# Kernel tuning notes

Hardware: AMD Instinct MI355X
Metric: run time of the kernel (lower is better)

The kernel has to match this reference:

```python
import jax, jax.numpy as jnp
import numpy as np

N_NODES = 50000
N_EDGES = 600000
N_GRAPHS = 512
D_IN = 128
D_H = 128
D_OUT = 10
N_LAYERS = 3
BN_EPS = 1e-5


def setup_inputs() -> dict:
    key = jax.random.key(0)
    ks = jax.random.split(key, 16)
    x = jax.random.normal(ks[0], (N_NODES, D_IN), dtype=jnp.float32)
    edge_index = jax.random.randint(ks[1], (2, N_EDGES), 0, N_NODES)
    # deterministic sorted batch assignment -> every graph non-empty
    batch = (jnp.arange(N_NODES) * N_GRAPHS) // N_NODES
    s = 1.0 / np.sqrt(D_H)
    w_in = jax.random.normal(ks[2], (D_IN, D_H), dtype=jnp.float32) * s
    b_in = jnp.zeros((D_H,), jnp.float32)
    conv_w = jax.random.normal(ks[3], (N_LAYERS, D_H, D_H), dtype=jnp.float32) * s
    conv_b = jnp.zeros((N_LAYERS, D_H), jnp.float32)
    bn_g = jnp.ones((N_LAYERS, D_H), jnp.float32)
    bn_b = jnp.zeros((N_LAYERS, D_H), jnp.float32)
    fc1_w = jax.random.normal(ks[4], (2 * D_H, D_H), dtype=jnp.float32) * (1.0 / np.sqrt(2 * D_H))
    fc1_b = jnp.zeros((D_H,), jnp.float32)
    fc2_w = jax.random.normal(ks[5], (D_H, D_OUT), dtype=jnp.float32) * s
    fc2_b = jnp.zeros((D_OUT,), jnp.float32)
    return {"x": x, "edge_index": edge_index, "batch": batch, "n_graphs": N_GRAPHS,
            "w_in": w_in, "b_in": b_in, "conv_w": conv_w, "conv_b": conv_b,
            "bn_g": bn_g, "bn_b": bn_b, "fc1_w": fc1_w, "fc1_b": fc1_b,
            "fc2_w": fc2_w, "fc2_b": fc2_b}


def reference(x, edge_index, batch, n_graphs, w_in, b_in, conv_w, conv_b,
              bn_g, bn_b, fc1_w, fc1_b, fc2_w, fc2_b):
    n = x.shape[0]
    loop = jnp.arange(n)
    src = jnp.concatenate([edge_index[0], loop])  # self-loops as in PyG GCNConv
    dst = jnp.concatenate([edge_index[1], loop])
    deg = jax.ops.segment_sum(jnp.ones_like(dst, x.dtype), dst, num_segments=n)
    dinv = jax.lax.rsqrt(deg)  # deg >= 1 due to self-loops
    enorm = dinv[src] * dinv[dst]  # (E+N,)

    h = jax.nn.relu(x @ w_in + b_in)
    for i in range(N_LAYERS):
        res = h
        m = h @ conv_w[i]
        # gather -> scale -> scatter-add (symmetric-normalized GCN propagation)
        m = jax.ops.segment_sum(m[src] * enorm[:, None], dst, num_segments=n) + conv_b[i]
        # batchnorm (training-mode batch statistics)
        mu = jnp.mean(m, axis=0)
        var = jnp.mean(jnp.square(m - mu), axis=0)
        m = (m - mu) * jax.lax.rsqrt(var + BN_EPS) * bn_g[i] + bn_b[i]
        m = jax.nn.relu(m)  # dropout is identity in eval
        h = m + res if i > 0 else m

    cnt = jax.ops.segment_sum(jnp.ones((n,), h.dtype), batch, num_segments=n_graphs)
    g_mean = jax.ops.segment_sum(h, batch, num_segments=n_graphs) / cnt[:, None]
    g_max = jax.ops.segment_max(h, batch, num_segments=n_graphs)
    g = jnp.concatenate([g_mean, g_max], axis=1)  # (G, 2*D_H)
    g = jax.nn.relu(g @ fc1_w + fc1_b)
    return g @ fc2_w + fc2_b
```

## Files before the change

### kernel.cpp

```cpp
#include <hip/hip_runtime.h>
#include <hip/hip_bf16.h>
#include <hip/hip_fp16.h>

#define N_NODES 50000
#define N_EDGES 600000
#define N_GRAPHS 512
#define DH 128
#define SLOTS 64
#define NCOPY 8

typedef __attribute__((ext_vector_type(8))) short bf16x8;
typedef __attribute__((ext_vector_type(4))) float fx4;
typedef __attribute__((ext_vector_type(8))) _Float16 hx8;

__device__ __forceinline__ short f2b(float f) {
    union { __hip_bfloat16 b; short s; } u;
    u.b = __float2bfloat16(f);
    return u.s;
}

__global__ void k_fill(const int* __restrict__ src, const int* __restrict__ dst,
                       int* __restrict__ fill, int* __restrict__ csr) {
    int e = blockIdx.x * 256 + threadIdx.x;
    if (e < N_EDGES) {
        int v = dst[e];
        int pos = atomicAdd(&fill[v], 1);
        if (pos < SLOTS) csr[v * SLOTS + pos] = src[e];
    }
}

__global__ void k_dinv(const int* __restrict__ fill, float* __restrict__ dinv) {
    int v = blockIdx.x * 256 + threadIdx.x;
    if (v < N_NODES) dinv[v] = rsqrtf((float)(fill[v] + 1));
}

__global__ void k_wcvt(const float* __restrict__ w_in, const float* __restrict__ conv_w,
                       __hip_bfloat16* __restrict__ Wp) {
    int id = blockIdx.x * 256 + threadIdx.x;
    if (id >= 4 * DH * DH) return;
    int mat = id >> 14, rem = id & 16383;
    int n = rem >> 7, k = rem & 127;
    const float* s = (mat == 0) ? w_in : (conv_w + (mat - 1) * DH * DH);
    Wp[id] = __float2bfloat16(s[k * DH + n]);
}

template <int MODE>
__global__ __launch_bounds__(256) void k_gemm(const float* __restrict__ A,
                                              const __hip_bfloat16* __restrict__ Wp,
                                              const float* __restrict__ bias,
                                              const float* __restrict__ coef,
                                              float* __restrict__ Hout,
                                              void* __restrict__ Cv) {
    int wave = blockIdx.x * 4 + (threadIdx.x >> 6);
    if (wave >= N_NODES / 16) return;
    int lane = threadIdx.x & 63;
    int r = lane & 15, gq = lane >> 4;
    const int row0 = wave * 16;

    const short* wp = (const short*)Wp;
    bf16x8 Bf[8][4];
#pragma unroll
    for (int t = 0; t < 8; ++t)
#pragma unroll
        for (int q = 0; q < 4; ++q)
            Bf[t][q] = *(const bf16x8*)(wp + (t * 16 + r) * DH + q * 32 + gq * 8);

    fx4 acc[8];
#pragma unroll
    for (int t = 0; t < 8; ++t) acc[t] = (fx4){0.f, 0.f, 0.f, 0.f};

    const float* arow = A + (size_t)(row0 + r) * DH;
#pragma unroll
    for (int q = 0; q < 4; ++q) {
        const int cb = q * 32 + gq * 8;
        fx4 a0 = *(const fx4*)(arow + cb);
        fx4 a1 = *(const fx4*)(arow + cb + 4);
        if (MODE >= 2) {
            fx4 sA0 = *(const fx4*)(coef + cb);
            fx4 sA1 = *(const fx4*)(coef + cb + 4);
            fx4 sB0 = *(const fx4*)(coef + DH + cb);
            fx4 sB1 = *(const fx4*)(coef + DH + cb + 4);
#pragma unroll
            for (int j = 0; j < 4; ++j) {
                a0[j] = fmaxf(a0[j] * sA0[j] + sB0[j], 0.f);
                a1[j] = fmaxf(a1[j] * sA1[j] + sB1[j], 0.f);
            }
            if (MODE == 3) {
                float* hrow = Hout + (size_t)(row0 + r) * DH + cb;
                a0 += *(const fx4*)(hrow);
                a1 += *(const fx4*)(hrow + 4);
            }
            float* hrow = Hout + (size_t)(row0 + r) * DH + cb;
            *(fx4*)(hrow) = a0;
            *(fx4*)(hrow + 4) = a1;
        }
        bf16x8 af;
        af[0] = f2b(a0[0]); af[1] = f2b(a0[1]); af[2] = f2b(a0[2]); af[3] = f2b(a0[3]);
        af[4] = f2b(a1[0]); af[5] = f2b(a1[1]); af[6] = f2b(a1[2]); af[7] = f2b(a1[3]);
#pragma unroll
        for (int t = 0; t < 8; ++t)
            acc[t] = __builtin_amdgcn_mfma_f32_16x16x32_bf16(af, Bf[t][q], acc[t], 0, 0, 0);
    }
#pragma unroll
    for (int t = 0; t < 8; ++t) {
#pragma unroll
        for (int rr = 0; rr < 4; ++rr) {
            int orow = row0 + 4 * gq + rr;
            int ocol = t * 16 + r;
            float v = acc[t][rr];
            if (MODE == 0) {
                v += bias[ocol];
                ((float*)Cv)[(size_t)orow * DH + ocol] = fmaxf(v, 0.f);
            } else {
                ((_Float16*)Cv)[(size_t)orow * DH + ocol] = (_Float16)v;
            }
        }
    }
}

__global__ __launch_bounds__(256) void k_prop(const _Float16* __restrict__ m,
                                              const int* __restrict__ csr,
                                              const int* __restrict__ deg,
                                              const float* __restrict__ dinv,
                                              float* __restrict__ agg,
                                              float* __restrict__ sums) {
    int g = threadIdx.x >> 4;
    int lane = threadIdx.x & 15;
    int v = blockIdx.x * 16 + g;
    float dv = dinv[v];
    hx8 self = ((const hx8*)(m + (size_t)v * DH))[lane];
    float acc[8];
#pragma unroll
    for (int j = 0; j < 8; ++j) acc[j] = dv * (float)self[j];
    int d = deg[v]; if (d > SLOTS) d = SLOTS;
    const int* nb = csr + (size_t)v * SLOTS;
    int i = 0;
    for (; i + 1 < d; i += 2) {
        int u0 = nb[i], u1 = nb[i + 1];
        float d0 = dinv[u0], d1 = dinv[u1];
        hx8 r0 = ((const hx8*)(m + (size_t)u0 * DH))[lane];
        hx8 r1 = ((const hx8*)(m + (size_t)u1 * DH))[lane];
#pragma unroll
        for (int j = 0; j < 8; ++j) acc[j] += d0 * (float)r0[j] + d1 * (float)r1[j];
    }
    if (i < d) {
        int u = nb[i];
        float du = dinv[u];
        hx8 ru = ((const hx8*)(m + (size_t)u * DH))[lane];
#pragma unroll
        for (int j = 0; j < 8; ++j) acc[j] += du * (float)ru[j];
    }
    float s[8], q2[8];
#pragma unroll
    for (int j = 0; j < 8; ++j) {
        float o = dv * acc[j];
        acc[j] = o;
        s[j] = o;
        q2[j] = o * o;
    }
    fx4 o0, o1;
#pragma unroll
    for (int j = 0; j < 4; ++j) { o0[j] = acc[j]; o1[j] = acc[4 + j]; }
    fx4* orow = (fx4*)(agg + (size_t)v * DH);
    orow[lane * 2] = o0;
    orow[lane * 2 + 1] = o1;

#pragma unroll
    for (int j = 0; j < 8; ++j) {
        s[j] += __shfl_xor(s[j], 16);
        s[j] += __shfl_xor(s[j], 32);
        q2[j] += __shfl_xor(q2[j], 16);
        q2[j] += __shfl_xor(q2[j], 32);
    }
    __shared__ float lsum[4][DH], lsq[4][DH];
    int wv = threadIdx.x >> 6, wl = threadIdx.x & 63;
    if (wl < 16) {
#pragma unroll
        for (int j = 0; j < 8; ++j) {
            lsum[wv][wl * 8 + j] = s[j];
            lsq[wv][wl * 8 + j] = q2[j];
        }
    }
    __syncthreads();
    if (threadIdx.x < DH) {
        int c = threadIdx.x;
        float ts = lsum[0][c] + lsum[1][c] + lsum[2][c] + lsum[3][c];
        float tq = lsq[0][c] + lsq[1][c] + lsq[2][c] + lsq[3][c];
        float* dstp = sums + (blockIdx.x & (NCOPY - 1)) * 256;
        atomicAdd(&dstp[c], ts);
        atomicAdd(&dstp[DH + c], tq);
    }
}

__global__ void k_bnfin(const float* __restrict__ sums, const float* __restrict__ gamma,
                        const float* __restrict__ beta, float* __restrict__ coef) {
    int c = threadIdx.x;
    if (c >= DH) return;
    float s = 0.f, q = 0.f;
    for (int k = 0; k < NCOPY; ++k) { s += sums[k * 256 + c]; q += sums[k * 256 + DH + c]; }
    const float invn = 1.f / (float)N_NODES;
    float mean = s * invn;
    float var = q * invn - mean * mean;
    float sA = gamma[c] * rsqrtf(var + 1e-5f);
    coef[c] = sA;
    coef[DH + c] = beta[c] - mean * sA;
}

__global__ __launch_bounds__(256) void k_pool(const float* __restrict__ agg,
                                              const float* __restrict__ coef,
                                              const float* __restrict__ hres,
                                              float* __restrict__ g) {
    int gr = blockIdx.x;
    int start = (gr * N_NODES + N_GRAPHS - 1) / N_GRAPHS;
    int end = ((gr + 1) * N_NODES + N_GRAPHS - 1) / N_GRAPHS;
    int grp = threadIdx.x >> 5, c4 = threadIdx.x & 31;
    fx4 sA = ((const fx4*)coef)[c4];
    fx4 sB = ((const fx4*)(coef + DH))[c4];
    fx4 sm = (fx4){0.f, 0.f, 0.f, 0.f};
    fx4 mx = (fx4){-3.4e38f, -3.4e38f, -3.4e38f, -3.4e38f};
    for (int v = start + grp; v < end; v += 8) {
        fx4 a = ((const fx4*)(agg + (size_t)v * DH))[c4];
        fx4 r = ((const fx4*)(hres + (size_t)v * DH))[c4];
        fx4 hv;
#pragma unroll
        for (int j = 0; j < 4; ++j) hv[j] = fmaxf(a[j] * sA[j] + sB[j], 0.f) + r[j];
        sm += hv;
#pragma unroll
        for (int j = 0; j < 4; ++j) mx[j] = fmaxf(mx[j], hv[j]);
    }
    __shared__ fx4 lsm[8][32], lmx[8][32];
    lsm[grp][c4] = sm;
    lmx[grp][c4] = mx;
    __syncthreads();
    if (threadIdx.x < 32) {
        int c = threadIdx.x;
        fx4 tsm = lsm[0][c], tmx = lmx[0][c];
#pragma unroll
        for (int k = 1; k < 8; ++k) {
            tsm += lsm[k][c];
#pragma unroll
            for (int j = 0; j < 4; ++j) tmx[j] = fmaxf(tmx[j], lmx[k][c][j]);
        }
        float inv = 1.f / (float)(end - start);
        tsm *= inv;
        *(fx4*)(g + gr * 256 + c * 4) = tsm;
        *(fx4*)(g + gr * 256 + DH + c * 4) = tmx;
    }
}

__global__ void k_head(const float* __restrict__ g, const float* __restrict__ fc1w,
                       const float* __restrict__ fc1b, const float* __restrict__ fc2w,
                       const float* __restrict__ fc2b, float* __restrict__ out) {
    __shared__ float tt[DH];
    int gr = blockIdx.x, j = threadIdx.x;
    const float* grow = g + gr * 256;
    float acc = fc1b[j];
    for (int k = 0; k < 256; ++k) acc += grow[k] * fc1w[k * DH + j];
    tt[j] = fmaxf(acc, 0.f);
    __syncthreads();
    if (j < 10) {
        float o = fc2b[j];
        for (int k = 0; k < DH; ++k) o += tt[k] * fc2w[k * 10 + j];
        out[gr * 10 + j] = o;
    }
}

extern "C" void kernel_launch(void* const* d_in, const int* in_sizes, int n_in,
                              void* d_out, int out_size, void* d_ws, size_t ws_size,
                              hipStream_t stream) {
    const float* x      = (const float*)d_in[0];
    const int*   ei     = (const int*)d_in[1];
    const float* w_in   = (const float*)d_in[4];
    const float* b_in   = (const float*)d_in[5];
    const float* conv_w = (const float*)d_in[6];
    const float* bn_g   = (const float*)d_in[8];
    const float* bn_b   = (const float*)d_in[9];
    const float* fc1w   = (const float*)d_in[10];
    const float* fc1b   = (const float*)d_in[11];
    const float* fc2w   = (const float*)d_in[12];
    const float* fc2b   = (const float*)d_in[13];
    float* out = (float*)d_out;

    const int* e_src = ei;
    const int* e_dst = ei + N_EDGES;

    char* ws = (char*)d_ws;
    size_t o = 0;
    auto alloc = [&](size_t bytes) { size_t r = o; o += (bytes + 255) & ~(size_t)255; return r; };
    size_t o_fill   = alloc(N_NODES * 4);
    size_t o_bnsum  = alloc(3 * NCOPY * 256 * 4);
    size_t zero_end = o;
    size_t o_dinv   = alloc(N_NODES * 4);
    size_t o_csr    = alloc((size_t)N_NODES * SLOTS * 4);
    size_t o_coef   = alloc(3 * 256 * 4);
    size_t o_wp     = alloc(4 * DH * DH * 2);
    size_t o_g      = alloc(N_GRAPHS * 256 * 4);
    size_t o_h      = alloc((size_t)N_NODES * DH * 4);
    size_t o_m      = alloc((size_t)N_NODES * DH * 2);
    size_t o_agg    = alloc((size_t)N_NODES * DH * 4);
    (void)ws_size;

    int*   fill   = (int*)(ws + o_fill);
    float* bnsum  = (float*)(ws + o_bnsum);
    float* dinv   = (float*)(ws + o_dinv);
    int*   csr    = (int*)(ws + o_csr);
    float* coef   = (float*)(ws + o_coef);
    __hip_bfloat16* wp = (__hip_bfloat16*)(ws + o_wp);
    float* gbuf   = (float*)(ws + o_g);
    float* h      = (float*)(ws + o_h);
    _Float16* m   = (_Float16*)(ws + o_m);
    float* agg    = (float*)(ws + o_agg);

    hipMemsetAsync(ws, 0, zero_end, stream);

    k_fill<<<(N_EDGES + 255) / 256, 256, 0, stream>>>(e_src, e_dst, fill, csr);
    k_dinv<<<(N_NODES + 255) / 256, 256, 0, stream>>>(fill, dinv);
    k_wcvt<<<(4 * DH * DH + 255) / 256, 256, 0, stream>>>(w_in, conv_w, wp);

    const int gemm_blocks = (N_NODES / 16 + 3) / 4;

    k_gemm<0><<<gemm_blocks, 256, 0, stream>>>(x, wp, b_in, nullptr, nullptr, h);

    k_gemm<1><<<gemm_blocks, 256, 0, stream>>>(h, wp + 1 * DH * DH, nullptr, nullptr, nullptr, m);
    k_prop<<<N_NODES / 16, 256, 0, stream>>>(m, csr, fill, dinv, agg, bnsum);
    k_bnfin<<<1, DH, 0, stream>>>(bnsum, bn_g, bn_b, coef);

    k_gemm<2><<<gemm_blocks, 256, 0, stream>>>(agg, wp + 2 * DH * DH, nullptr, coef, h, m);
    k_prop<<<N_NODES / 16, 256, 0, stream>>>(m, csr, fill, dinv, agg, bnsum + NCOPY * 256);
    k_bnfin<<<1, DH, 0, stream>>>(bnsum + NCOPY * 256, bn_g + DH, bn_b + DH, coef + 256);

    k_gemm<3><<<gemm_blocks, 256, 0, stream>>>(agg, wp + 3 * DH * DH, nullptr, coef + 256, h, m);
    k_prop<<<N_NODES / 16, 256, 0, stream>>>(m, csr, fill, dinv, agg, bnsum + 2 * NCOPY * 256);
    k_bnfin<<<1, DH, 0, stream>>>(bnsum + 2 * NCOPY * 256, bn_g + 2 * DH, bn_b + 2 * DH, coef + 512);

    k_pool<<<N_GRAPHS, 256, 0, stream>>>(agg, coef + 512, h, gbuf);
    k_head<<<N_GRAPHS, DH, 0, stream>>>(gbuf, fc1w, fc1b, fc2w, fc2b, out);
}
```

Before: 351.2 us.

## Store h and agg in fp16, fold bnfin into prop, merge setup kernels

The intermediate node feature buffers h and agg switch from fp32 to fp16, which halves the memory traffic in the gemm, prop and pool kernels. The BN finalize step moves into the last block of each prop launch through an atomic ticket. The fill and weight-convert kernels merge into one launch, and dinv is now recomputed inline from the degrees. The prop gather is unrolled by 4 with int4 neighbour loads. The main costs are lower precision in the residual stream and extra rsqrt work per neighbour.

Result: slower. 1.215 ms (+245.8%).

```diff
diff --git a/kernel.cpp b/kernel.cpp
--- a/kernel.cpp
+++ b/kernel.cpp
@@ -8,6 +8,9 @@
 #define DH 128
 #define SLOTS 64
 #define NCOPY 8
+#define FILL_BLOCKS ((N_EDGES + 255) / 256)
+#define WCVT_BLOCKS ((4 * DH * DH) / 256)
+#define PROP_BLOCKS (N_NODES / 16)
 
 typedef __attribute__((ext_vector_type(8))) short bf16x8;
 typedef __attribute__((ext_vector_type(4))) float fx4;
@@ -19,38 +22,34 @@
     return u.s;
 }
 
-__global__ void k_fill(const int* __restrict__ src, const int* __restrict__ dst,
-                       int* __restrict__ fill, int* __restrict__ csr) {
-    int e = blockIdx.x * 256 + threadIdx.x;
-    if (e < N_EDGES) {
-        int v = dst[e];
-        int pos = atomicAdd(&fill[v], 1);
-        if (pos < SLOTS) csr[v * SLOTS + pos] = src[e];
-    }
-}
-
-__global__ void k_dinv(const int* __restrict__ fill, float* __restrict__ dinv) {
-    int v = blockIdx.x * 256 + threadIdx.x;
-    if (v < N_NODES) dinv[v] = rsqrtf((float)(fill[v] + 1));
-}
-
-__global__ void k_wcvt(const float* __restrict__ w_in, const float* __restrict__ conv_w,
-                       __hip_bfloat16* __restrict__ Wp) {
-    int id = blockIdx.x * 256 + threadIdx.x;
-    if (id >= 4 * DH * DH) return;
-    int mat = id >> 14, rem = id & 16383;
-    int n = rem >> 7, k = rem & 127;
-    const float* s = (mat == 0) ? w_in : (conv_w + (mat - 1) * DH * DH);
-    Wp[id] = __float2bfloat16(s[k * DH + n]);
+__global__ void k_build(const int* __restrict__ src, const int* __restrict__ dst,
+                        int* __restrict__ fill, int* __restrict__ csr,
+                        const float* __restrict__ w_in, const float* __restrict__ conv_w,
+                        __hip_bfloat16* __restrict__ Wp) {
+    int b = blockIdx.x;
+    if (b < FILL_BLOCKS) {
+        int e = b * 256 + threadIdx.x;
+        if (e < N_EDGES) {
+            int v = dst[e];
+            int pos = atomicAdd(&fill[v], 1);
+            if (pos < SLOTS) csr[v * SLOTS + pos] = src[e];
+        }
+    } else {
+        int id = (b - FILL_BLOCKS) * 256 + threadIdx.x;
+        int mat = id >> 14, rem = id & 16383;
+        int n = rem >> 7, k = rem & 127;
+        const float* s = (mat == 0) ? w_in : (conv_w + (mat - 1) * DH * DH);
+        Wp[id] = __float2bfloat16(s[k * DH + n]);
+    }
 }
 
 template <int MODE>
-__global__ __launch_bounds__(256) void k_gemm(const float* __restrict__ A,
+__global__ __launch_bounds__(256) void k_gemm(const void* __restrict__ Av,
                                               const __hip_bfloat16* __restrict__ Wp,
                                               const float* __restrict__ bias,
                                               const float* __restrict__ coef,
-                                              float* __restrict__ Hout,
-                                              void* __restrict__ Cv) {
+                                              _Float16* __restrict__ Hout,
+                                              _Float16* __restrict__ Cm) {
     int wave = blockIdx.x * 4 + (threadIdx.x >> 6);
     if (wave >= N_NODES / 16) return;
     int lane = threadIdx.x & 63;
@@ -69,12 +68,22 @@
 #pragma unroll
     for (int t = 0; t < 8; ++t) acc[t] = (fx4){0.f, 0.f, 0.f, 0.f};
 
-    const float* arow = A + (size_t)(row0 + r) * DH;
 #pragma unroll
     for (int q = 0; q < 4; ++q) {
         const int cb = q * 32 + gq * 8;
-        fx4 a0 = *(const fx4*)(arow + cb);
-        fx4 a1 = *(const fx4*)(arow + cb + 4);
+        float a[8];
+        if (MODE == 0) {
+            const float* arow = (const float*)Av + (size_t)(row0 + r) * DH + cb;
+            fx4 a0 = *(const fx4*)(arow);
+            fx4 a1 = *(const fx4*)(arow + 4);
+#pragma unroll
+            for (int j = 0; j < 4; ++j) { a[j] = a0[j]; a[4 + j] = a1[j]; }
+        } else {
+            const _Float16* arow = (const _Float16*)Av + (size_t)(row0 + r) * DH + cb;
+            hx8 av = *(const hx8*)(arow);
+#pragma unroll
+            for (int j = 0; j < 8; ++j) a[j] = (float)av[j];
+        }
         if (MODE >= 2) {
             fx4 sA0 = *(const fx4*)(coef + cb);
             fx4 sA1 = *(const fx4*)(coef + cb + 4);
@@ -82,21 +91,23 @@
             fx4 sB1 = *(const fx4*)(coef + DH + cb + 4);
 #pragma unroll
             for (int j = 0; j < 4; ++j) {
-                a0[j] = fmaxf(a0[j] * sA0[j] + sB0[j], 0.f);
-                a1[j] = fmaxf(a1[j] * sA1[j] + sB1[j], 0.f);
+                a[j]     = fmaxf(a[j] * sA0[j] + sB0[j], 0.f);
+                a[4 + j] = fmaxf(a[4 + j] * sA1[j] + sB1[j], 0.f);
             }
+            _Float16* hrow = Hout + (size_t)(row0 + r) * DH + cb;
             if (MODE == 3) {
-                float* hrow = Hout + (size_t)(row0 + r) * DH + cb;
-                a0 += *(const fx4*)(hrow);
-                a1 += *(const fx4*)(hrow + 4);
+                hx8 rv = *(const hx8*)hrow;
+#pragma unroll
+                for (int j = 0; j < 8; ++j) a[j] += (float)rv[j];
             }
-            float* hrow = Hout + (size_t)(row0 + r) * DH + cb;
-            *(fx4*)(hrow) = a0;
-            *(fx4*)(hrow + 4) = a1;
+            hx8 hv;
+#pragma unroll
+            for (int j = 0; j < 8; ++j) hv[j] = (_Float16)a[j];
+            *(hx8*)hrow = hv;
         }
         bf16x8 af;
-        af[0] = f2b(a0[0]); af[1] = f2b(a0[1]); af[2] = f2b(a0[2]); af[3] = f2b(a0[3]);
-        af[4] = f2b(a1[0]); af[5] = f2b(a1[1]); af[6] = f2b(a1[2]); af[7] = f2b(a1[3]);
+#pragma unroll
+        for (int j = 0; j < 8; ++j) af[j] = f2b(a[j]);
 #pragma unroll
         for (int t = 0; t < 8; ++t)
             acc[t] = __builtin_amdgcn_mfma_f32_16x16x32_bf16(af, Bf[t][q], acc[t], 0, 0, 0);
@@ -108,12 +119,8 @@
             int orow = row0 + 4 * gq + rr;
             int ocol = t * 16 + r;
             float v = acc[t][rr];
-            if (MODE == 0) {
-                v += bias[ocol];
-                ((float*)Cv)[(size_t)orow * DH + ocol] = fmaxf(v, 0.f);
-            } else {
-                ((_Float16*)Cv)[(size_t)orow * DH + ocol] = (_Float16)v;
-            }
+            if (MODE == 0) v = fmaxf(v + bias[ocol], 0.f);
+            Cm[(size_t)orow * DH + ocol] = (_Float16)v;
         }
     }
 }
@@ -121,49 +128,55 @@
 __global__ __launch_bounds__(256) void k_prop(const _Float16* __restrict__ m,
                                               const int* __restrict__ csr,
                                               const int* __restrict__ deg,
-                                              const float* __restrict__ dinv,
-                                              float* __restrict__ agg,
-                                              float* __restrict__ sums) {
+                                              _Float16* __restrict__ agg,
+                                              float* __restrict__ sums,
+                                              const float* __restrict__ gamma,
+                                              const float* __restrict__ beta,
+                                              float* __restrict__ coef,
+                                              int* __restrict__ ticket) {
     int g = threadIdx.x >> 4;
     int lane = threadIdx.x & 15;
     int v = blockIdx.x * 16 + g;
-    float dv = dinv[v];
+    int dvi = deg[v];
+    float dv = rsqrtf((float)(dvi + 1));
     hx8 self = ((const hx8*)(m + (size_t)v * DH))[lane];
     float acc[8];
 #pragma unroll
     for (int j = 0; j < 8; ++j) acc[j] = dv * (float)self[j];
-    int d = deg[v]; if (d > SLOTS) d = SLOTS;
+    int d = dvi > SLOTS ? SLOTS : dvi;
     const int* nb = csr + (size_t)v * SLOTS;
     int i = 0;
-    for (; i + 1 < d; i += 2) {
-        int u0 = nb[i], u1 = nb[i + 1];
-        float d0 = dinv[u0], d1 = dinv[u1];
-        hx8 r0 = ((const hx8*)(m + (size_t)u0 * DH))[lane];
-        hx8 r1 = ((const hx8*)(m + (size_t)u1 * DH))[lane];
-#pragma unroll
-        for (int j = 0; j < 8; ++j) acc[j] += d0 * (float)r0[j] + d1 * (float)r1[j];
-    }
-    if (i < d) {
+    for (; i + 3 < d; i += 4) {
+        int4 uu = *(const int4*)(nb + i);
+        float e0 = rsqrtf((float)(deg[uu.x] + 1));
+        float e1 = rsqrtf((float)(deg[uu.y] + 1));
+        float e2 = rsqrtf((float)(deg[uu.z] + 1));
+        float e3 = rsqrtf((float)(deg[uu.w] + 1));
+        hx8 r0 = ((const hx8*)(m + (size_t)uu.x * DH))[lane];
+        hx8 r1 = ((const hx8*)(m + (size_t)uu.y * DH))[lane];
+        hx8 r2 = ((const hx8*)(m + (size_t)uu.z * DH))[lane];
+        hx8 r3 = ((const hx8*)(m + (size_t)uu.w * DH))[lane];
+#pragma unroll
+        for (int j = 0; j < 8; ++j)
+            acc[j] += e0 * (float)r0[j] + e1 * (float)r1[j] + e2 * (float)r2[j] + e3 * (float)r3[j];
+    }
+    for (; i < d; ++i) {
         int u = nb[i];
-        float du = dinv[u];
+        float eu = rsqrtf((float)(deg[u] + 1));
         hx8 ru = ((const hx8*)(m + (size_t)u * DH))[lane];
 #pragma unroll
-        for (int j = 0; j < 8; ++j) acc[j] += du * (float)ru[j];
+        for (int j = 0; j < 8; ++j) acc[j] += eu * (float)ru[j];
     }
     float s[8], q2[8];
+    hx8 ov;
 #pragma unroll
     for (int j = 0; j < 8; ++j) {
         float o = dv * acc[j];
-        acc[j] = o;
+        ov[j] = (_Float16)o;
         s[j] = o;
         q2[j] = o * o;
     }
-    fx4 o0, o1;
-#pragma unroll
-    for (int j = 0; j < 4; ++j) { o0[j] = acc[j]; o1[j] = acc[4 + j]; }
-    fx4* orow = (fx4*)(agg + (size_t)v * DH);
-    orow[lane * 2] = o0;
-    orow[lane * 2 + 1] = o1;
+    ((hx8*)(agg + (size_t)v * DH))[lane] = ov;
 
 #pragma unroll
     for (int j = 0; j < 8; ++j) {
@@ -173,6 +186,7 @@
         q2[j] += __shfl_xor(q2[j], 32);
     }
     __shared__ float lsum[4][DH], lsq[4][DH];
+    __shared__ int lastf;
     int wv = threadIdx.x >> 6, wl = threadIdx.x & 63;
     if (wl < 16) {
 #pragma unroll
@@ -190,61 +204,78 @@
         atomicAdd(&dstp[c], ts);
         atomicAdd(&dstp[DH + c], tq);
     }
-}
-
-__global__ void k_bnfin(const float* __restrict__ sums, const float* __restrict__ gamma,
-                        const float* __restrict__ beta, float* __restrict__ coef) {
-    int c = threadIdx.x;
-    if (c >= DH) return;
-    float s = 0.f, q = 0.f;
-    for (int k = 0; k < NCOPY; ++k) { s += sums[k * 256 + c]; q += sums[k * 256 + DH + c]; }
-    const float invn = 1.f / (float)N_NODES;
-    float mean = s * invn;
-    float var = q * invn - mean * mean;
-    float sA = gamma[c] * rsqrtf(var + 1e-5f);
-    coef[c] = sA;
-    coef[DH + c] = beta[c] - mean * sA;
-}
-
-__global__ __launch_bounds__(256) void k_pool(const float* __restrict__ agg,
+    __threadfence();
+    __syncthreads();
+    if (threadIdx.x == 0) lastf = (atomicAdd(ticket, 1) == PROP_BLOCKS - 1);
+    __syncthreads();
+    if (lastf && threadIdx.x < DH) {
+        int c = threadIdx.x;
+        __threadfence();
+        float ss = 0.f, qq = 0.f;
+        for (int k = 0; k < NCOPY; ++k) {
+            ss += atomicAdd(&sums[k * 256 + c], 0.f);
+            qq += atomicAdd(&sums[k * 256 + DH + c], 0.f);
+        }
+        const float invn = 1.f / (float)N_NODES;
+        float mean = ss * invn;
+        float var = qq * invn - mean * mean;
+        float sA = gamma[c] * rsqrtf(var + 1e-5f);
+        coef[c] = sA;
+        coef[DH + c] = beta[c] - mean * sA;
+    }
+}
+
+__global__ __launch_bounds__(256) void k_pool(const _Float16* __restrict__ agg,
                                               const float* __restrict__ coef,
-                                              const float* __restrict__ hres,
+                                              const _Float16* __restrict__ hres,
                                               float* __restrict__ g) {
     int gr = blockIdx.x;
     int start = (gr * N_NODES + N_GRAPHS - 1) / N_GRAPHS;
     int end = ((gr + 1) * N_NODES + N_GRAPHS - 1) / N_GRAPHS;
-    int grp = threadIdx.x >> 5, c4 = threadIdx.x & 31;
-    fx4 sA = ((const fx4*)coef)[c4];
-    fx4 sB = ((const fx4*)(coef + DH))[c4];
-    fx4 sm = (fx4){0.f, 0.f, 0.f, 0.f};
-    fx4 mx = (fx4){-3.4e38f, -3.4e38f, -3.4e38f, -3.4e38f};
-    for (int v = start + grp; v < end; v += 8) {
-        fx4 a = ((const fx4*)(agg + (size_t)v * DH))[c4];
-        fx4 r = ((const fx4*)(hres + (size_t)v * DH))[c4];
-        fx4 hv;
-#pragma unroll
-        for (int j = 0; j < 4; ++j) hv[j] = fmaxf(a[j] * sA[j] + sB[j], 0.f) + r[j];
-        sm += hv;
-#pragma unroll
-        for (int j = 0; j < 4; ++j) mx[j] = fmaxf(mx[j], hv[j]);
-    }
-    __shared__ fx4 lsm[8][32], lmx[8][32];
-    lsm[grp][c4] = sm;
-    lmx[grp][c4] = mx;
-    __syncthreads();
-    if (threadIdx.x < 32) {
+    int grp = threadIdx.x >> 4, lane = threadIdx.x & 15;
+    fx4 cA0 = ((const fx4*)coef)[lane * 2];
+    fx4 cA1 = ((const fx4*)coef)[lane * 2 + 1];
+    fx4 cB0 = ((const fx4*)(coef + DH))[lane * 2];
+    fx4 cB1 = ((const fx4*)(coef + DH))[lane * 2 + 1];
+    float sA[8], sB[8];
+#pragma unroll
+    for (int j = 0; j < 4; ++j) { sA[j] = cA0[j]; sA[4 + j] = cA1[j]; sB[j] = cB0[j]; sB[4 + j] = cB1[j]; }
+    float sm[8], mx[8];
+#pragma unroll
+    for (int j = 0; j < 8; ++j) { sm[j] = 0.f; mx[j] = -3.4e38f; }
+    for (int v = start + grp; v < end; v += 16) {
+        hx8 a = ((const hx8*)(agg + (size_t)v * DH))[lane];
+        hx8 r = ((const hx8*)(hres + (size_t)v * DH))[lane];
+#pragma unroll
+        for (int j = 0; j < 8; ++j) {
+            float hv = fmaxf((float)a[j] * sA[j] + sB[j], 0.f) + (float)r[j];
+            sm[j] += hv;
+            mx[j] = fmaxf(mx[j], hv);
+        }
+    }
+#pragma unroll
+    for (int j = 0; j < 8; ++j) {
+        sm[j] += __shfl_xor(sm[j], 16);
+        sm[j] += __shfl_xor(sm[j], 32);
+        mx[j] = fmaxf(mx[j], __shfl_xor(mx[j], 16));
+        mx[j] = fmaxf(mx[j], __shfl_xor(mx[j], 32));
+    }
+    __shared__ float psum[4][DH], pmax[4][DH];
+    int wv = threadIdx.x >> 6, wl = threadIdx.x & 63;
+    if (wl < 16) {
+#pragma unroll
+        for (int j = 0; j < 8; ++j) {
+            psum[wv][wl * 8 + j] = sm[j];
+            pmax[wv][wl * 8 + j] = mx[j];
+        }
+    }
+    __syncthreads();
+    if (threadIdx.x < DH) {
         int c = threadIdx.x;
-        fx4 tsm = lsm[0][c], tmx = lmx[0][c];
-#pragma unroll
-        for (int k = 1; k < 8; ++k) {
-            tsm += lsm[k][c];
-#pragma unroll
-            for (int j = 0; j < 4; ++j) tmx[j] = fmaxf(tmx[j], lmx[k][c][j]);
-        }
-        float inv = 1.f / (float)(end - start);
-        tsm *= inv;
-        *(fx4*)(g + gr * 256 + c * 4) = tsm;
-        *(fx4*)(g + gr * 256 + DH + c * 4) = tmx;
+        float ts = psum[0][c] + psum[1][c] + psum[2][c] + psum[3][c];
+        float tm = fmaxf(fmaxf(pmax[0][c], pmax[1][c]), fmaxf(pmax[2][c], pmax[3][c]));
+        g[gr * 256 + c] = ts / (float)(end - start);
+        g[gr * 256 + DH + c] = tm;
     }
 }
 
@@ -289,49 +320,48 @@
     auto alloc = [&](size_t bytes) { size_t r = o; o += (bytes + 255) & ~(size_t)255; return r; };
     size_t o_fill   = alloc(N_NODES * 4);
     size_t o_bnsum  = alloc(3 * NCOPY * 256 * 4);
+    size_t o_tick   = alloc(3 * 4);
     size_t zero_end = o;
-    size_t o_dinv   = alloc(N_NODES * 4);
     size_t o_csr    = alloc((size_t)N_NODES * SLOTS * 4);
     size_t o_coef   = alloc(3 * 256 * 4);
     size_t o_wp     = alloc(4 * DH * DH * 2);
     size_t o_g      = alloc(N_GRAPHS * 256 * 4);
-    size_t o_h      = alloc((size_t)N_NODES * DH * 4);
+    size_t o_h      = alloc((size_t)N_NODES * DH * 2);
     size_t o_m      = alloc((size_t)N_NODES * DH * 2);
-    size_t o_agg    = alloc((size_t)N_NODES * DH * 4);
+    size_t o_agg    = alloc((size_t)N_NODES * DH * 2);
     (void)ws_size;
 
     int*   fill   = (int*)(ws + o_fill);
     float* bnsum  = (float*)(ws + o_bnsum);
-    float* dinv   = (float*)(ws + o_dinv);
+    int*   tick   = (int*)(ws + o_tick);
     int*   csr    = (int*)(ws + o_csr);
     float* coef   = (float*)(ws + o_coef);
     __hip_bfloat16* wp = (__hip_bfloat16*)(ws + o_wp);
     float* gbuf   = (float*)(ws + o_g);
-    float* h      = (float*)(ws + o_h);
+    _Float16* h   = (_Float16*)(ws + o_h);
     _Float16* m   = (_Float16*)(ws + o_m);
-    float* agg    = (float*)(ws + o_agg);
+    _Float16* agg = (_Float16*)(ws + o_agg);
 
     hipMemsetAsync(ws, 0, zero_end, stream);
 
-    k_fill<<<(N_EDGES + 255) / 256, 256, 0, stream>>>(e_src, e_dst, fill, csr);
-    k_dinv<<<(N_NODES + 255) / 256, 256, 0, stream>>>(fill, dinv);
-    k_wcvt<<<(4 * DH * DH + 255) / 256, 256, 0, stream>>>(w_in, conv_w, wp);
+    k_build<<<FILL_BLOCKS + WCVT_BLOCKS, 256, 0, stream>>>(e_src, e_dst, fill, csr,
+                                                           w_in, conv_w, wp);
 
     const int gemm_blocks = (N_NODES / 16 + 3) / 4;
 
     k_gemm<0><<<gemm_blocks, 256, 0, stream>>>(x, wp, b_in, nullptr, nullptr, h);
 
     k_gemm<1><<<gemm_blocks, 256, 0, stream>>>(h, wp + 1 * DH * DH, nullptr, nullptr, nullptr, m);
-    k_prop<<<N_NODES / 16, 256, 0, stream>>>(m, csr, fill, dinv, agg, bnsum);
-    k_bnfin<<<1, DH, 0, stream>>>(bnsum, bn_g, bn_b, coef);
+    k_prop<<<PROP_BLOCKS, 256, 0, stream>>>(m, csr, fill, agg, bnsum,
+                                            bn_g, bn_b, coef, tick);
 
     k_gemm<2><<<gemm_blocks, 256, 0, stream>>>(agg, wp + 2 * DH * DH, nullptr, coef, h, m);
-    k_prop<<<N_NODES / 16, 256, 0, stream>>>(m, csr, fill, dinv, agg, bnsum + NCOPY * 256);
-    k_bnfin<<<1, DH, 0, stream>>>(bnsum + NCOPY * 256, bn_g + DH, bn_b + DH, coef + 256);
+    k_prop<<<PROP_BLOCKS, 256, 0, stream>>>(m, csr, fill, agg, bnsum + NCOPY * 256,
+                                            bn_g + DH, bn_b + DH, coef + 256, tick + 1);
 
     k_gemm<3><<<gemm_blocks, 256, 0, stream>>>(agg, wp + 3 * DH * DH, nullptr, coef + 256, h, m);
-    k_prop<<<N_NODES / 16, 256, 0, stream>>>(m, csr, fill, dinv, agg, bnsum + 2 * NCOPY * 256);
-    k_bnfin<<<1, DH, 0, stream>>>(bnsum + 2 * NCOPY * 256, bn_g + 2 * DH, bn_b + 2 * DH, coef + 512);
+    k_prop<<<PROP_BLOCKS, 256, 0, stream>>>(m, csr, fill, agg, bnsum + 2 * NCOPY * 256,
+                                            bn_g + 2 * DH, bn_b + 2 * DH, coef + 512, tick + 2);
 
     k_pool<<<N_GRAPHS, 256, 0, stream>>>(agg, coef + 512, h, gbuf);
     k_head<<<N_GRAPHS, DH, 0, stream>>>(gbuf, fc1w, fc1b, fc2w, fc2b, out);
```
